# Kernel optimization log

Measured on AMD Instinct MI355X. Metric: run time of the kernel, lower is better.

Reference implementation:

```python
import jax, jax.numpy as jnp
import numpy as np

TEMP = 0.1
LAM = 1.0
NORM_EPS = 1e-12   # torch F.normalize eps
COS_EPS = 1e-8     # torch F.cosine_similarity eps


def l2norm(x, axis):
    n = jnp.sqrt(jnp.sum(x * x, axis=axis, keepdims=True))
    return x / jnp.maximum(n, NORM_EPS)


def cos_sim(a, b, axis):
    na = jnp.sqrt(jnp.sum(a * a, axis=axis))
    nb = jnp.sqrt(jnp.sum(b * b, axis=axis))
    return jnp.sum(a * b, axis=axis) / jnp.maximum(na * nb, COS_EPS)


def setup_inputs() -> dict:
    key = jax.random.key(0)
    k1, k2, k3, k4, k5 = jax.random.split(key, 5)
    B, C, H, W = 32, 256, 32, 32
    return {
        "q_b": jax.random.normal(k1, (B, C, H, W), dtype=jnp.float32),
        "k_b": jax.random.normal(k2, (B, C, H, W), dtype=jnp.float32),
        "q_grid": jax.random.normal(k3, (B, C, H, W), dtype=jnp.float32),
        "k_grid": jax.random.normal(k4, (B, C, H, W), dtype=jnp.float32),
        "labels": jax.random.randint(k5, (B,), 0, 10, dtype=jnp.int64),
    }


def densecl(q_b, k_b, q_grid, k_grid, labels):
    B, C, H, W = q_b.shape
    S = H * W
    q_b = l2norm(q_b, axis=1)
    k_b = l2norm(k_b, axis=1)
    q_grid = l2norm(q_grid, axis=1)
    k_grid = l2norm(k_grid, axis=1)

    q_b_flat = q_b.reshape(B, C, S)
    k_b_flat = k_b.reshape(B, C, S)
    # spatial correspondence: [B, S, S]
    sim = jnp.einsum('bci,bcj->bij', q_b_flat, k_b_flat)
    max_sim_idx = jnp.argmax(sim, axis=-1)  # [B, S]

    Cg = q_grid.shape[1]
    q_grid_flat = q_grid.reshape(B, Cg, S)
    k_grid_flat = k_grid.reshape(B, Cg, S)
    idx = jnp.broadcast_to(max_sim_idx[:, None, :], (B, Cg, S))
    k_matched = jnp.take_along_axis(k_grid_flat, idx, axis=2)
    pos_sim = cos_sim(q_grid_flat, k_matched, axis=1) / TEMP  # [B, S]

    # random negative from a different-label sample (use_prototypes=False path)
    key = jax.random.key(42)
    u = jax.random.uniform(key, (B, B))
    mask = labels[:, None] != labels[None, :]
    neg_idx = jnp.argmax(jnp.where(mask, u, -1.0), axis=1)  # [B]
    neg_k = k_grid_flat[neg_idx]  # [B, Cg, S]
    neg_sim = cos_sim(q_grid_flat, neg_k, axis=1) / TEMP  # [B, S]

    loss = -jnp.log(jnp.exp(pos_sim) / (jnp.exp(pos_sim) + jnp.exp(neg_sim) + 1e-6))
    return jnp.mean(loss)


def reference(q_b, k_b, q_grid, k_grid, labels):
    return densecl(q_b, k_b, q_grid, k_grid, labels) * LAM
```

## Files before the change

kernel.cpp:

```cpp
#include <hip/hip_runtime.h>
#include <hip/hip_bf16.h>
#include <math.h>
#include <stdint.h>

#define BB 32
#define CC 256
#define SS 1024

typedef __attribute__((ext_vector_type(8))) short short8v;
typedef __attribute__((ext_vector_type(4))) float f32x4;

#define ASYNC16(g, l)                                                        \
  __builtin_amdgcn_global_load_lds(                                          \
      (const __attribute__((address_space(1))) void*)(g),                    \
      (__attribute__((address_space(3))) void*)(l), 16, 0, 0)

__device__ __forceinline__ unsigned short bf16_rne(float f) {
  unsigned int u = __float_as_uint(f);
  unsigned int r = (u + 0x7fffu + ((u >> 16) & 1u)) >> 16;
  return (unsigned short)r;
}

__device__ __forceinline__ void tf_round(uint32_t& x0, uint32_t& x1, int r) {
  x0 += x1;
  x1 = (x1 << r) | (x1 >> (32 - r));
  x1 ^= x0;
}

__device__ __forceinline__ void tf_gen(int t, float* u) {
  uint32_t x0 = (uint32_t)t;
  uint32_t x1 = (uint32_t)(t + 512);
  const uint32_t ks0 = 0u, ks1 = 42u, ks2 = 0x1BD11BDAu ^ 0u ^ 42u;
  x0 += ks0; x1 += ks1;
  tf_round(x0, x1, 13); tf_round(x0, x1, 15); tf_round(x0, x1, 26); tf_round(x0, x1, 6);
  x0 += ks1; x1 += ks2 + 1u;
  tf_round(x0, x1, 17); tf_round(x0, x1, 29); tf_round(x0, x1, 16); tf_round(x0, x1, 24);
  x0 += ks2; x1 += ks0 + 2u;
  tf_round(x0, x1, 13); tf_round(x0, x1, 15); tf_round(x0, x1, 26); tf_round(x0, x1, 6);
  x0 += ks0; x1 += ks1 + 3u;
  tf_round(x0, x1, 17); tf_round(x0, x1, 29); tf_round(x0, x1, 16); tf_round(x0, x1, 24);
  x0 += ks1; x1 += ks2 + 4u;
  tf_round(x0, x1, 13); tf_round(x0, x1, 15); tf_round(x0, x1, 26); tf_round(x0, x1, 6);
  x0 += ks2; x1 += ks0 + 5u;
  u[t]       = __uint_as_float((x0 >> 9) | 0x3f800000u) - 1.0f;
  u[t + 512] = __uint_as_float((x1 >> 9) | 0x3f800000u) - 1.0f;
}

__global__ __launch_bounds__(256, 4) void transnorm_kernel(
    const float* __restrict__ qb, const float* __restrict__ kb,
    const float* __restrict__ kg, unsigned short* __restrict__ qt,
    unsigned short* __restrict__ kt, unsigned short* __restrict__ kgt,
    float* __restrict__ invqb, float* __restrict__ invkb,
    float* __restrict__ invkg, const int* __restrict__ labels,
    int* __restrict__ negidx, unsigned long long* __restrict__ best,
    float* __restrict__ out) {
  const int bid = blockIdx.x;
  const int tid = threadIdx.x;

  __shared__ unsigned int tile[64 * 128];
  __shared__ float part[16][65];

  if (bid >= 1536) {
    if (bid == 1536) {
      float* u = (float*)&tile[0];
      tf_gen(tid, u);
      tf_gen(tid + 256, u);
      if (tid == 0) *out = 0.f;
      __syncthreads();
      if (tid < BB) {
        int lb = labels[tid];
        float bestv = -1.0f;
        int bj = 0;
        for (int j = 0; j < BB; ++j) {
          float v = (labels[j] != lb) ? u[tid * BB + j] : -1.0f;
          if (v > bestv) { bestv = v; bj = j; }
        }
        negidx[tid] = bj;
      }
    } else {
      unsigned long long* bp = best + (size_t)(bid - 1537) * 8192 + tid;
#pragma unroll
      for (int i = 0; i < 32; ++i) bp[(size_t)i * 256] = 0ull;
    }
    return;
  }

  const int which = bid >> 9;
  const int sub = bid & 511;
  const int b = sub >> 4;
  const int s0 = (sub & 15) * 64;

  const float* src = (which == 0) ? qb : (which == 1) ? kb : kg;
  unsigned short* dst = (which == 0) ? qt : (which == 1) ? kt : kgt;
  float* inv = (which == 0) ? invqb : (which == 1) ? invkb : invkg;

  const int sg = tid & 15;
  const int cq = tid >> 4;

  const float* sp = src + (size_t)b * CC * SS + s0 + sg * 4;
  float ssq[4] = {0.f, 0.f, 0.f, 0.f};

#pragma unroll
  for (int half = 0; half < 2; ++half) {
    float4 xa[4], xb[4];
#pragma unroll
    for (int kk = 0; kk < 4; ++kk) {
      int cp = cq + 16 * (half * 4 + kk);
      int c = cp * 2;
      xa[kk] = *(const float4*)(sp + ((size_t)c << 10));
      xb[kk] = *(const float4*)(sp + ((size_t)(c + 1) << 10));
    }
#pragma unroll
    for (int kk = 0; kk < 4; ++kk) {
      int cp = cq + 16 * (half * 4 + kk);
      float a[4] = {xa[kk].x, xa[kk].y, xa[kk].z, xa[kk].w};
      float bb[4] = {xb[kk].x, xb[kk].y, xb[kk].z, xb[kk].w};
#pragma unroll
      for (int e = 0; e < 4; ++e) {
        ssq[e] = fmaf(a[e], a[e], ssq[e]);
        ssq[e] = fmaf(bb[e], bb[e], ssq[e]);
        int r = sg * 4 + e;
        int colp = cp ^ (sg << 2);
        tile[r * 128 + colp] =
            (unsigned)bf16_rne(a[e]) | ((unsigned)bf16_rne(bb[e]) << 16);
      }
    }
  }
#pragma unroll
  for (int e = 0; e < 4; ++e) part[cq][sg * 4 + e] = ssq[e];
  __syncthreads();

  const int h = tid >> 5, cw = tid & 31;
  unsigned short* dp = dst + ((size_t)b * SS + s0) * CC;
#pragma unroll
  for (int p = 0; p < 8; ++p) {
    int r = p * 8 + h;
    int colb = (cw * 4) ^ ((r >> 2) << 2);
    uint4 pk = *(const uint4*)&tile[r * 128 + colb];
    *(uint4*)(dp + (size_t)r * CC + cw * 8) = pk;
  }
  if (tid < 64) {
    float s = 0.f;
#pragma unroll
    for (int k = 0; k < 16; ++k) s += part[k][tid];
    inv[b * SS + s0 + tid] = 1.0f / fmaxf(sqrtf(s), 1e-12f);
  }
}

__device__ __forceinline__ void sim_stage(
    const unsigned short* __restrict__ aG, const unsigned short* __restrict__ bG,
    unsigned short* SA, unsigned short* SB, int ch, int w, int r8, int p) {
#pragma unroll
  for (int v = 0; v < 4; ++v) {
    int r = v * 32 + w * 8 + r8;
    int clog = p ^ (r & 7);
    ASYNC16(aG + (size_t)r * CC + ch * 64 + clog * 8, &SA[(v * 32 + w * 8) * 64]);
    ASYNC16(bG + (size_t)r * CC + ch * 64 + clog * 8, &SB[(v * 32 + w * 8) * 64]);
  }
}

__device__ __forceinline__ void sim_compute(
    const unsigned short* SA, const unsigned short* SB, f32x4 acc[4][4],
    int wi, int wj, int q4, int m16) {
#pragma unroll
  for (int kk = 0; kk < 2; ++kk) {
    short8v af[4], bf[4];
#pragma unroll
    for (int mt = 0; mt < 4; ++mt) {
      int i = wi + mt * 16 + m16;
      int cp = (kk * 4 + q4) ^ (i & 7);
      af[mt] = *(const short8v*)&SA[i * 64 + cp * 8];
      int j = wj + mt * 16 + m16;
      int cq = (kk * 4 + q4) ^ (j & 7);
      bf[mt] = *(const short8v*)&SB[j * 64 + cq * 8];
    }
#pragma unroll
    for (int mt = 0; mt < 4; ++mt)
#pragma unroll
      for (int nt = 0; nt < 4; ++nt)
        acc[mt][nt] = __builtin_amdgcn_mfma_f32_16x16x32_bf16(
            af[mt], bf[nt], acc[mt][nt], 0, 0, 0);
  }
}

__global__ __launch_bounds__(256, 2) void simargmax_mfma(
    const unsigned short* __restrict__ qt, const unsigned short* __restrict__ kt,
    const float* __restrict__ invk, unsigned long long* __restrict__ best) {
  const int bid0 = blockIdx.x;
  const int W = (bid0 & 7) * 256 + (bid0 >> 3);
  const int b = W >> 6, it = (W >> 3) & 7, jt = W & 7;
  const int t = threadIdx.x, w = t >> 6, l = t & 63;

  __shared__ unsigned short sa0[128 * 64];
  __shared__ unsigned short sa1[128 * 64];
  __shared__ unsigned short sb0[128 * 64];
  __shared__ unsigned short sb1[128 * 64];
  __shared__ unsigned long long cand2[128][2];
  __shared__ float sinvk[128];

  if (t < 128) sinvk[t] = invk[b * SS + jt * 128 + t];

  const unsigned short* aG = qt + ((size_t)b * SS + it * 128) * CC;
  const unsigned short* bG = kt + ((size_t)b * SS + jt * 128) * CC;

  f32x4 acc[4][4];
#pragma unroll
  for (int mt = 0; mt < 4; ++mt)
#pragma unroll
    for (int nt = 0; nt < 4; ++nt) acc[mt][nt] = (f32x4){0.f, 0.f, 0.f, 0.f};

  const int r8 = l >> 3, p = l & 7;
  const int q4 = l >> 4, m16 = l & 15;
  const int wi = (w >> 1) * 64, wj = (w & 1) * 64;

  sim_stage(aG, bG, sa0, sb0, 0, w, r8, p);
  __syncthreads();
  sim_stage(aG, bG, sa1, sb1, 1, w, r8, p);
  sim_compute(sa0, sb0, acc, wi, wj, q4, m16);
  __syncthreads();
  sim_stage(aG, bG, sa0, sb0, 2, w, r8, p);
  sim_compute(sa1, sb1, acc, wi, wj, q4, m16);
  __syncthreads();
  sim_stage(aG, bG, sa1, sb1, 3, w, r8, p);
  sim_compute(sa0, sb0, acc, wi, wj, q4, m16);
  __syncthreads();
  sim_compute(sa1, sb1, acc, wi, wj, q4, m16);

  float siv[4];
#pragma unroll
  for (int nt = 0; nt < 4; ++nt) siv[nt] = sinvk[wj + nt * 16 + m16];

  unsigned long long bp[4][4];
#pragma unroll
  for (int mt = 0; mt < 4; ++mt) {
#pragma unroll
    for (int e = 0; e < 4; ++e) {
      unsigned long long mx = 0ull;
#pragma unroll
      for (int nt = 0; nt < 4; ++nt) {
        float v = acc[mt][nt][e] * siv[nt];
        unsigned int u = __float_as_uint(v);
        u = (u & 0x80000000u) ? ~u : (u | 0x80000000u);
        int col = jt * 128 + wj + nt * 16 + m16;
        unsigned long long pk =
            ((unsigned long long)u << 32) | (unsigned)(1023 - col);
        mx = (pk > mx) ? pk : mx;
      }
      bp[mt][e] = mx;
    }
  }
#pragma unroll
  for (int d = 1; d < 16; d <<= 1) {
#pragma unroll
    for (int mt = 0; mt < 4; ++mt)
#pragma unroll
      for (int e = 0; e < 4; ++e) {
        unsigned long long o = __shfl_xor(bp[mt][e], d, 64);
        if (o > bp[mt][e]) bp[mt][e] = o;
      }
  }
  if (m16 == 0) {
#pragma unroll
    for (int mt = 0; mt < 4; ++mt)
#pragma unroll
      for (int e = 0; e < 4; ++e)
        cand2[wi + mt * 16 + q4 * 4 + e][w & 1] = bp[mt][e];
  }
  __syncthreads();
  if (t < 128) {
    unsigned long long m0 = cand2[t][0], m1 = cand2[t][1];
    atomicMax(&best[b * SS + it * 128 + t], m0 > m1 ? m0 : m1);
  }
}

__global__ void negidx_kernel(const int* __restrict__ labels, int* __restrict__ negidx) {
  __shared__ float u[1024];
  int t = threadIdx.x;
  tf_gen(t, u);
  __syncthreads();
  if (t < BB) {
    int lb = labels[t];
    float bestv = -1.0f;
    int bj = 0;
    for (int j = 0; j < BB; ++j) {
      float v = (labels[j] != lb) ? u[t * BB + j] : -1.0f;
      if (v > bestv) { bestv = v; bj = j; }
    }
    negidx[t] = bj;
  }
}

__global__ __launch_bounds__(256) void loss_fused_kernel(
    const float* __restrict__ qg, const unsigned short* __restrict__ kgt,
    const float* __restrict__ invkg, const unsigned long long* __restrict__ best,
    const int* __restrict__ negidx, float* __restrict__ out) {
  const int tid = threadIdx.x;
  const int s_l = tid & 31, g = tid >> 5;
  const int P0 = blockIdx.x * 32;
  const int b = P0 >> 10;
  const int s = (P0 & (SS - 1)) + s_l;
  const int idx = b * SS + s;
  const int js = 1023 - (int)(best[idx] & 0xffffffffu);
  const int nb = negidx[b];

  const float* qcol = qg + ((size_t)b * CC + g * 32) * SS + s;
  const unsigned short* kp = kgt + ((size_t)b * SS + js) * CC + g * 32;
  const unsigned short* kn = kgt + ((size_t)nb * SS + s) * CC + g * 32;

  float dp = 0.f, dn = 0.f, sq = 0.f;
#pragma unroll
  for (int uu = 0; uu < 4; ++uu) {
    uint4 up = *(const uint4*)(kp + uu * 8);
    uint4 un = *(const uint4*)(kn + uu * 8);
    float q[8];
#pragma unroll
    for (int j = 0; j < 8; ++j) {
      q[j] = qcol[(size_t)(uu * 8 + j) << 10];
      sq = fmaf(q[j], q[j], sq);
    }
    float pv[8], nv[8];
    pv[0] = __uint_as_float(up.x << 16); pv[1] = __uint_as_float(up.x & 0xffff0000u);
    pv[2] = __uint_as_float(up.y << 16); pv[3] = __uint_as_float(up.y & 0xffff0000u);
    pv[4] = __uint_as_float(up.z << 16); pv[5] = __uint_as_float(up.z & 0xffff0000u);
    pv[6] = __uint_as_float(up.w << 16); pv[7] = __uint_as_float(up.w & 0xffff0000u);
    nv[0] = __uint_as_float(un.x << 16); nv[1] = __uint_as_float(un.x & 0xffff0000u);
    nv[2] = __uint_as_float(un.y << 16); nv[3] = __uint_as_float(un.y & 0xffff0000u);
    nv[4] = __uint_as_float(un.z << 16); nv[5] = __uint_as_float(un.z & 0xffff0000u);
    nv[6] = __uint_as_float(un.w << 16); nv[7] = __uint_as_float(un.w & 0xffff0000u);
#pragma unroll
    for (int j = 0; j < 8; ++j) {
      dp = fmaf(q[j], pv[j], dp);
      dn = fmaf(q[j], nv[j], dn);
    }
  }

  __shared__ float rdp[8][33], rdn[8][33], rsq[8][33];
  rdp[g][s_l] = dp;
  rdn[g][s_l] = dn;
  rsq[g][s_l] = sq;
  __syncthreads();
  if (tid < 32) {
    float DP = 0.f, DN = 0.f, SQ = 0.f;
#pragma unroll
    for (int k = 0; k < 8; ++k) {
      DP += rdp[k][tid];
      DN += rdn[k][tid];
      SQ += rsq[k][tid];
    }
    int s2 = (P0 & (SS - 1)) + tid;
    int idx2 = b * SS + s2;
    int js2 = 1023 - (int)(best[idx2] & 0xffffffffu);
    float iq = 1.0f / fmaxf(sqrtf(SQ), 1e-12f);
    float pvv = DP * iq * invkg[b * SS + js2] * 10.0f;
    float nvv = DN * iq * invkg[nb * SS + s2] * 10.0f;
    float elem = logf(expf(pvv) + expf(nvv) + 1e-6f) - pvv;
#pragma unroll
    for (int o = 16; o > 0; o >>= 1) elem += __shfl_down(elem, o, 32);
    if (tid == 0) atomicAdd(out, elem * (1.0f / (BB * SS)));
  }
}

__global__ __launch_bounds__(256) void norms_kernel(
    const float* __restrict__ qb, const float* __restrict__ kb,
    const float* __restrict__ qg, const float* __restrict__ kg,
    float* __restrict__ inv) {
  int t = blockIdx.x * 256 + threadIdx.x;
  int which = t >> 15;
  int bs = t & (BB * SS - 1);
  const float* src = (which == 0) ? qb : (which == 1) ? kb : (which == 2) ? qg : kg;
  int b = bs >> 10;
  int s = bs & (SS - 1);
  const float* p = src + (size_t)b * CC * SS + s;
  float ss = 0.f;
#pragma unroll 8
  for (int c = 0; c < CC; ++c) {
    float x = p[(size_t)c * SS];
    ss = fmaf(x, x, ss);
  }
  float n = fmaxf(sqrtf(ss), 1e-12f);
  inv[t] = 1.0f / n;
}

#define TI 64
#define TJ 128
#define KC 32

__global__ __launch_bounds__(256) void simargmax_kernel(
    const float* __restrict__ qb, const float* __restrict__ kb,
    const float* __restrict__ invq, const float* __restrict__ invk,
    int* __restrict__ amax) {
  const int b = blockIdx.x >> 4;
  const int i0 = (blockIdx.x & 15) * TI;
  const int t = threadIdx.x;
  const int ti = t >> 4;
  const int tj = t & 15;

  __shared__ float aQ[KC][TI];
  __shared__ float bK[KC][TJ];
  __shared__ float redv[TI][16];
  __shared__ int redj[TI][16];

  const float* qbase = qb + (size_t)b * CC * SS + i0;
  const float* kbase = kb + (size_t)b * CC * SS;
  const float* ivq = invq + b * SS + i0;
  const float* ivk = invk + b * SS;

  float best_v = -3.4e38f;
  int best_j = 0;

  for (int j0 = 0; j0 < SS; j0 += TJ) {
    float acc[4][8];
#pragma unroll
    for (int r = 0; r < 4; ++r)
#pragma unroll
      for (int rr = 0; rr < 8; ++rr) acc[r][rr] = 0.f;

    for (int c0 = 0; c0 < CC; c0 += KC) {
      __syncthreads();
#pragma unroll
      for (int v = 0; v < 2; ++v) {
        int f = t + v * 256;
        int cl = f >> 4;
        int sl = (f & 15) << 2;
        float4 qa = *(const float4*)(qbase + (size_t)(c0 + cl) * SS + sl);
        float4 iv = *(const float4*)(ivq + sl);
        aQ[cl][sl + 0] = qa.x * iv.x;
        aQ[cl][sl + 1] = qa.y * iv.y;
        aQ[cl][sl + 2] = qa.z * iv.z;
        aQ[cl][sl + 3] = qa.w * iv.w;
      }
#pragma unroll
      for (int v = 0; v < 4; ++v) {
        int f = t + v * 256;
        int cl = f >> 5;
        int sl = (f & 31) << 2;
        float4 ka = *(const float4*)(kbase + (size_t)(c0 + cl) * SS + j0 + sl);
        float4 ik = *(const float4*)(ivk + j0 + sl);
        bK[cl][sl + 0] = ka.x * ik.x;
        bK[cl][sl + 1] = ka.y * ik.y;
        bK[cl][sl + 2] = ka.z * ik.z;
        bK[cl][sl + 3] = ka.w * ik.w;
      }
      __syncthreads();
#pragma unroll
      for (int kc = 0; kc < KC; ++kc) {
        float4 a0 = *(const float4*)&aQ[kc][ti * 4];
        float4 b0 = *(const float4*)&bK[kc][tj * 8];
        float4 b1 = *(const float4*)&bK[kc][tj * 8 + 4];
        float av[4] = {a0.x, a0.y, a0.z, a0.w};
        float bv[8] = {b0.x, b0.y, b0.z, b0.w, b1.x, b1.y, b1.z, b1.w};
#pragma unroll
        for (int r = 0; r < 4; ++r)
#pragma unroll
          for (int rr = 0; rr < 8; ++rr)
            acc[r][rr] = fmaf(av[r], bv[rr], acc[r][rr]);
      }
    }
    __syncthreads();
#pragma unroll
    for (int r = 0; r < 4; ++r) {
      float v = acc[r][0];
      int jb = j0 + tj * 8;
#pragma unroll
      for (int rr = 1; rr < 8; ++rr) {
        if (acc[r][rr] > v) { v = acc[r][rr]; jb = j0 + tj * 8 + rr; }
      }
      redv[ti * 4 + r][tj] = v;
      redj[ti * 4 + r][tj] = jb;
    }
    __syncthreads();
    if (t < TI) {
#pragma unroll
      for (int ww = 0; ww < 16; ++ww) {
        float v = redv[t][ww];
        if (v > best_v) { best_v = v; best_j = redj[t][ww]; }
      }
    }
  }
  if (t < TI) amax[b * SS + i0 + t] = best_j;
}

__global__ __launch_bounds__(256) void loss_kernel(
    const float* __restrict__ qg, const float* __restrict__ kg,
    const float* __restrict__ invq, const float* __restrict__ invk,
    const int* __restrict__ amax, const int* __restrict__ negidx,
    float* __restrict__ out) {
  int t = blockIdx.x * 256 + threadIdx.x;
  int b = t >> 10;
  int s = t & (SS - 1);
  int js = amax[t];
  int nb = negidx[b];
  const float* qcol = qg + (size_t)b * CC * SS + s;
  const float* kpcol = kg + (size_t)b * CC * SS + js;
  const float* kncol = kg + (size_t)nb * CC * SS + s;
  float dp = 0.f, dn = 0.f;
#pragma unroll 8
  for (int c = 0; c < CC; ++c) {
    float q = qcol[(size_t)c * SS];
    dp = fmaf(q, kpcol[(size_t)c * SS], dp);
    dn = fmaf(q, kncol[(size_t)c * SS], dn);
  }
  float iq = invq[t];
  float pv = dp * iq * invk[b * SS + js] * 10.0f;
  float nv = dn * iq * invk[nb * SS + s] * 10.0f;
  float elem = logf(expf(pv) + expf(nv) + 1e-6f) - pv;

  __shared__ float red[256];
  red[threadIdx.x] = elem;
  __syncthreads();
  for (int o = 128; o > 0; o >>= 1) {
    if (threadIdx.x < o) red[threadIdx.x] += red[threadIdx.x + o];
    __syncthreads();
  }
  if (threadIdx.x == 0) atomicAdd(out, red[0] * (1.0f / (BB * SS)));
}

extern "C" void kernel_launch(void* const* d_in, const int* in_sizes, int n_in,
                              void* d_out, int out_size, void* d_ws, size_t ws_size,
                              hipStream_t stream) {
  const float* qb = (const float*)d_in[0];
  const float* kb = (const float*)d_in[1];
  const float* qg = (const float*)d_in[2];
  const float* kg = (const float*)d_in[3];
  const int* labels = (const int*)d_in[4];

  char* ws = (char*)d_ws;
  float* invqb = (float*)ws;
  float* invkb = (float*)(ws + 128 * 1024);
  float* invkg = (float*)(ws + 256 * 1024);
  unsigned long long* best = (unsigned long long*)(ws + 384 * 1024);
  int* negidx = (int*)(ws + 640 * 1024);
  unsigned short* qt = (unsigned short*)(ws + (1 << 20));
  unsigned short* kt = (unsigned short*)(ws + (17 << 20));
  unsigned short* kgt = (unsigned short*)(ws + (33 << 20));

  const size_t need = (size_t)49 * 1024 * 1024;
  const bool fast = ws_size >= need;

  if (fast) {
    transnorm_kernel<<<1541, 256, 0, stream>>>(qb, kb, kg, qt, kt, kgt, invqb,
                                               invkb, invkg, labels, negidx,
                                               best, (float*)d_out);
    simargmax_mfma<<<2048, 256, 0, stream>>>(qt, kt, invkb, best);
    loss_fused_kernel<<<1024, 256, 0, stream>>>(qg, kgt, invkg, best, negidx,
                                                (float*)d_out);
  } else {
    hipMemsetAsync(d_out, 0, sizeof(float), stream);
    float* inv = (float*)ws;
    int* amax = (int*)(ws + 512 * 1024);
    int* negidx2 = (int*)(ws + 640 * 1024);
    norms_kernel<<<(4 * BB * SS) / 256, 256, 0, stream>>>(qb, kb, qg, kg, inv);
    simargmax_kernel<<<BB * (SS / TI), 256, 0, stream>>>(
        qb, kb, inv + 0 * BB * SS, inv + 1 * BB * SS, amax);
    negidx_kernel<<<1, 512, 0, stream>>>(labels, negidx2);
    loss_kernel<<<(BB * SS) / 256, 256, 0, stream>>>(
        qg, kg, inv + 2 * BB * SS, inv + 3 * BB * SS, amax, negidx2,
        (float*)d_out);
  }
}
```

Before: 205.7 us.

## Interleave k_grid transpose-normalize blocks into the similarity/argmax kernel

The k_grid transpose, bf16 conversion and inverse-norm work moves out of the first kernel and into the MFMA similarity kernel, where every fifth block does one transnorm tile. The aim is to overlap this memory-bound work with the compute-bound matmul/argmax blocks and to shorten the first kernel. Shared memory is now one manually carved buffer, and the block-to-tile mapping is remapped to skip the interleaved blocks while keeping the XCD-aware ordering. The risks are extra index arithmetic and possible load imbalance or occupancy effects from mixing block types.

```diff
diff --git a/kernel.cpp b/kernel.cpp
--- a/kernel.cpp
+++ b/kernel.cpp
@@ -46,22 +46,78 @@
   u[t + 512] = __uint_as_float((x1 >> 9) | 0x3f800000u) - 1.0f;
 }
 
+__device__ __forceinline__ void tn_body(const float* __restrict__ src,
+                                        unsigned short* __restrict__ dst,
+                                        float* __restrict__ inv, int b, int s0,
+                                        int tid, unsigned int* tile,
+                                        float (*part)[65]) {
+  const int sg = tid & 15;
+  const int cq = tid >> 4;
+
+  const float* sp = src + (size_t)b * CC * SS + s0 + sg * 4;
+  float ssq[4] = {0.f, 0.f, 0.f, 0.f};
+
+#pragma unroll
+  for (int half = 0; half < 2; ++half) {
+    float4 xa[4], xb[4];
+#pragma unroll
+    for (int kk = 0; kk < 4; ++kk) {
+      int cp = cq + 16 * (half * 4 + kk);
+      int c = cp * 2;
+      xa[kk] = *(const float4*)(sp + ((size_t)c << 10));
+      xb[kk] = *(const float4*)(sp + ((size_t)(c + 1) << 10));
+    }
+#pragma unroll
+    for (int kk = 0; kk < 4; ++kk) {
+      int cp = cq + 16 * (half * 4 + kk);
+      float a[4] = {xa[kk].x, xa[kk].y, xa[kk].z, xa[kk].w};
+      float bb[4] = {xb[kk].x, xb[kk].y, xb[kk].z, xb[kk].w};
+#pragma unroll
+      for (int e = 0; e < 4; ++e) {
+        ssq[e] = fmaf(a[e], a[e], ssq[e]);
+        ssq[e] = fmaf(bb[e], bb[e], ssq[e]);
+        int r = sg * 4 + e;
+        int colp = cp ^ (sg << 2);
+        tile[r * 128 + colp] =
+            (unsigned)bf16_rne(a[e]) | ((unsigned)bf16_rne(bb[e]) << 16);
+      }
+    }
+  }
+#pragma unroll
+  for (int e = 0; e < 4; ++e) part[cq][sg * 4 + e] = ssq[e];
+  __syncthreads();
+
+  const int h = tid >> 5, cw = tid & 31;
+  unsigned short* dp = dst + ((size_t)b * SS + s0) * CC;
+#pragma unroll
+  for (int p = 0; p < 8; ++p) {
+    int r = p * 8 + h;
+    int colb = (cw * 4) ^ ((r >> 2) << 2);
+    uint4 pk = *(const uint4*)&tile[r * 128 + colb];
+    *(uint4*)(dp + (size_t)r * CC + cw * 8) = pk;
+  }
+  if (tid < 64) {
+    float s = 0.f;
+#pragma unroll
+    for (int k = 0; k < 16; ++k) s += part[k][tid];
+    inv[b * SS + s0 + tid] = 1.0f / fmaxf(sqrtf(s), 1e-12f);
+  }
+}
+
 __global__ __launch_bounds__(256, 4) void transnorm_kernel(
     const float* __restrict__ qb, const float* __restrict__ kb,
-    const float* __restrict__ kg, unsigned short* __restrict__ qt,
-    unsigned short* __restrict__ kt, unsigned short* __restrict__ kgt,
+    unsigned short* __restrict__ qt, unsigned short* __restrict__ kt,
     float* __restrict__ invqb, float* __restrict__ invkb,
-    float* __restrict__ invkg, const int* __restrict__ labels,
-    int* __restrict__ negidx, unsigned long long* __restrict__ best,
-    float* __restrict__ out) {
+    const int* __restrict__ labels, int* __restrict__ negidx,
+    unsigned long long* __restrict__ best, float* __restrict__ out) {
   const int bid = blockIdx.x;
   const int tid = threadIdx.x;
 
   __shared__ unsigned int tile[64 * 128];
   __shared__ float part[16][65];
 
-  if (bid >= 1536) {
-    if (bid == 1536) {
+  if (bid >= 1024) {
+    if (bid == 1024) {
       float* u = (float*)&tile[0];
       tf_gen(tid, u);
       tf_gen(tid + 256, u);
@@ -78,7 +134,7 @@
         negidx[tid] = bj;
       }
     } else {
-      unsigned long long* bp = best + (size_t)(bid - 1537) * 8192 + tid;
+      unsigned long long* bp = best + (size_t)(bid - 1025) * 8192 + tid;
 #pragma unroll
       for (int i = 0; i < 32; ++i) bp[(size_t)i * 256] = 0ull;
     }
@@ -87,64 +143,8 @@
 
   const int which = bid >> 9;
   const int sub = bid & 511;
-  const int b = sub >> 4;
-  const int s0 = (sub & 15) * 64;
-
-  const float* src = (which == 0) ? qb : (which == 1) ? kb : kg;
-  unsigned short* dst = (which == 0) ? qt : (which == 1) ? kt : kgt;
-  float* inv = (which == 0) ? invqb : (which == 1) ? invkb : invkg;
-
-  const int sg = tid & 15;
-  const int cq = tid >> 4;
-
-  const float* sp = src + (size_t)b * CC * SS + s0 + sg * 4;
-  float ssq[4] = {0.f, 0.f, 0.f, 0.f};
-
-#pragma unroll
-  for (int half = 0; half < 2; ++half) {
-    float4 xa[4], xb[4];
-#pragma unroll
-    for (int kk = 0; kk < 4; ++kk) {
-      int cp = cq + 16 * (half * 4 + kk);
-      int c = cp * 2;
-      xa[kk] = *(const float4*)(sp + ((size_t)c << 10));
-      xb[kk] = *(const float4*)(sp + ((size_t)(c + 1) << 10));
-    }
-#pragma unroll
-    for (int kk = 0; kk < 4; ++kk) {
-      int cp = cq + 16 * (half * 4 + kk);
-      float a[4] = {xa[kk].x, xa[kk].y, xa[kk].z, xa[kk].w};
-      float bb[4] = {xb[kk].x, xb[kk].y, xb[kk].z, xb[kk].w};
-#pragma unroll
-      for (int e = 0; e < 4; ++e) {
-        ssq[e] = fmaf(a[e], a[e], ssq[e]);
-        ssq[e] = fmaf(bb[e], bb[e], ssq[e]);
-        int r = sg * 4 + e;
-        int colp = cp ^ (sg << 2);
-        tile[r * 128 + colp] =
-            (unsigned)bf16_rne(a[e]) | ((unsigned)bf16_rne(bb[e]) << 16);
-      }
-    }
-  }
-#pragma unroll
-  for (int e = 0; e < 4; ++e) part[cq][sg * 4 + e] = ssq[e];
-  __syncthreads();
-
-  const int h = tid >> 5, cw = tid & 31;
-  unsigned short* dp = dst + ((size_t)b * SS + s0) * CC;
-#pragma unroll
-  for (int p = 0; p < 8; ++p) {
-    int r = p * 8 + h;
-    int colb = (cw * 4) ^ ((r >> 2) << 2);
-    uint4 pk = *(const uint4*)&tile[r * 128 + colb];
-    *(uint4*)(dp + (size_t)r * CC + cw * 8) = pk;
-  }
-  if (tid < 64) {
-    float s = 0.f;
-#pragma unroll
-    for (int k = 0; k < 16; ++k) s += part[k][tid];
-    inv[b * SS + s0 + tid] = 1.0f / fmaxf(sqrtf(s), 1e-12f);
-  }
+  tn_body(which ? kb : qb, which ? kt : qt, which ? invkb : invqb, sub >> 4,
+          (sub & 15) * 64, tid, tile, part);
 }
 
 __device__ __forceinline__ void sim_stage(
@@ -183,20 +183,38 @@
   }
 }
 
-__global__ __launch_bounds__(256, 2) void simargmax_mfma(
+__global__ __launch_bounds__(256, 2) void megasim_kernel(
     const unsigned short* __restrict__ qt, const unsigned short* __restrict__ kt,
-    const float* __restrict__ invk, unsigned long long* __restrict__ best) {
-  const int bid0 = blockIdx.x;
-  const int W = (bid0 & 7) * 256 + (bid0 >> 3);
+    const float* __restrict__ invk, unsigned long long* __restrict__ best,
+    const float* __restrict__ kg, unsigned short* __restrict__ kgt,
+    float* __restrict__ invkg) {
+  __shared__ __align__(16) char smem[68096];
+  const int bid = blockIdx.x;
+  const int t = threadIdx.x;
+
+  if ((bid % 5) == 4) {
+    const int tn_idx = bid / 5;
+    tn_body(kg, kgt, invkg, tn_idx >> 4, (tn_idx & 15) * 64, t,
+            (unsigned int*)smem, (float(*)[65])(smem + 32768));
+    return;
+  }
+
+  const int x = bid & 7;
+  const int k = ((bid % 40) - x) >> 3;
+  int o = 0;
+#pragma unroll
+  for (int kk = 0; kk < 4; ++kk)
+    if (kk < k && ((x + 8 * kk) % 5) != 4) ++o;
+  const int W = x * 256 + (bid / 40) * 4 + o;
   const int b = W >> 6, it = (W >> 3) & 7, jt = W & 7;
-  const int t = threadIdx.x, w = t >> 6, l = t & 63;
-
-  __shared__ unsigned short sa0[128 * 64];
-  __shared__ unsigned short sa1[128 * 64];
-  __shared__ unsigned short sb0[128 * 64];
-  __shared__ unsigned short sb1[128 * 64];
-  __shared__ unsigned long long cand2[128][2];
-  __shared__ float sinvk[128];
+  const int w = t >> 6, l = t & 63;
+
+  unsigned short* sa0 = (unsigned short*)(smem);
+  unsigned short* sa1 = (unsigned short*)(smem + 16384);
+  unsigned short* sb0 = (unsigned short*)(smem + 32768);
+  unsigned short* sb1 = (unsigned short*)(smem + 49152);
+  unsigned long long (*cand2)[2] = (unsigned long long(*)[2])(smem + 65536);
+  float* sinvk = (float*)(smem + 65536 + 2048);
 
   if (t < 128) sinvk[t] = invk[b * SS + jt * 128 + t];
 
@@ -255,8 +273,8 @@
     for (int mt = 0; mt < 4; ++mt)
 #pragma unroll
       for (int e = 0; e < 4; ++e) {
-        unsigned long long o = __shfl_xor(bp[mt][e], d, 64);
-        if (o > bp[mt][e]) bp[mt][e] = o;
+        unsigned long long o2 = __shfl_xor(bp[mt][e], d, 64);
+        if (o2 > bp[mt][e]) bp[mt][e] = o2;
       }
   }
   if (m16 == 0) {
@@ -538,10 +556,11 @@
   const bool fast = ws_size >= need;
 
   if (fast) {
-    transnorm_kernel<<<1541, 256, 0, stream>>>(qb, kb, kg, qt, kt, kgt, invqb,
-                                               invkb, invkg, labels, negidx,
-                                               best, (float*)d_out);
-    simargmax_mfma<<<2048, 256, 0, stream>>>(qt, kt, invkb, best);
+    transnorm_kernel<<<1029, 256, 0, stream>>>(qb, kb, qt, kt, invqb, invkb,
+                                               labels, negidx, best,
+                                               (float*)d_out);
+    megasim_kernel<<<2560, 256, 0, stream>>>(qt, kt, invkb, best, kg, kgt,
+                                             invkg);
     loss_fused_kernel<<<1024, 256, 0, stream>>>(qg, kgt, invkg, best, negidx,
                                                 (float*)d_out);
   } else {
```

New measurement: 201.0 us. 1.02x faster.
